# Kernel optimization log

Hardware: AMD Instinct MI355X
Metric: run time of the kernel (lower is better)

## Reference

```python
import jax, jax.numpy as jnp
import numpy as np

N = 50000       # nodes
E = 500000      # directed edges
Q_EDGES = 100000
F_IN = 128
HID = 64
K = 2           # Chebyshev order -> K+1 weight slices
LABEL = 2
Q_PHASE = 0.25
TWO_PI = 2.0 * np.pi


def setup_inputs() -> dict:
    key = jax.random.key(0)
    ks = jax.random.split(key, 9)
    real = jax.random.normal(ks[0], (N, F_IN), jnp.float32)
    imag = jax.random.normal(ks[1], (N, F_IN), jnp.float32)
    src = jax.random.randint(ks[2], (E,), 0, N)
    off = jax.random.randint(ks[3], (E,), 1, N)
    dst = (src + off) % N  # no self loops (torch code removes them)
    edge_index = jnp.stack([src, dst]).astype(jnp.int64)
    query_edges = jax.random.randint(ks[4], (Q_EDGES, 2), 0, N).astype(jnp.int64)
    edge_weight = jax.random.uniform(ks[5], (E,), jnp.float32, 0.5, 1.5)
    W1 = jax.random.normal(ks[6], (K + 1, F_IN, HID), jnp.float32) / np.sqrt(F_IN)
    b1 = jnp.zeros((HID,), jnp.float32)
    W2 = jax.random.normal(ks[7], (K + 1, HID, HID), jnp.float32) / np.sqrt(HID)
    b2 = jnp.zeros((HID,), jnp.float32)
    Wlin = jax.random.normal(ks[8], (LABEL, 4 * HID), jnp.float32) / np.sqrt(4 * HID)
    blin = jnp.zeros((LABEL,), jnp.float32)
    return dict(real=real, imag=imag, edge_index=edge_index, query_edges=query_edges,
                edge_weight=edge_weight, W1=W1, b1=b1, W2=W2, b2=b2, Wlin=Wlin, blin=blin)


def magnetic_norm(edge_index, edge_weight, num_nodes, q):
    """Edge weights of scaled magnetic Laplacian L_hat = L - I (sym norm, lambda_max=2).

    Returns symmetrized edge list (2E edges) with real/imag coefficients
    -D^{-1/2} A_s D^{-1/2} * exp(i * theta), theta = 2*pi*q*(A - A^T).
    """
    u, v = edge_index[0], edge_index[1]
    s = jnp.concatenate([u, v])                  # source (j)
    d = jnp.concatenate([v, u])                  # target (i)
    w_sym = jnp.concatenate([edge_weight, edge_weight]) * 0.5  # A_s = (A + A^T)/2
    theta = TWO_PI * q * jnp.concatenate([edge_weight, -edge_weight])
    deg = jax.ops.segment_sum(w_sym, s, num_segments=num_nodes)
    dinv = jnp.where(deg > 0, jax.lax.rsqrt(jnp.where(deg > 0, deg, 1.0)), 0.0)
    norm = dinv[s] * w_sym * dinv[d]
    return s, d, -norm * jnp.cos(theta), -norm * jnp.sin(theta)


def magnet_conv(xr, xi, s, d, nr, ni, W, b, num_nodes):
    def prop(x, c):  # out[i] = sum_{e: d_e = i} c_e * x[s_e]
        return jax.ops.segment_sum(c[:, None] * x[s], d, num_segments=num_nodes)

    xs = (xr, xi, xr, xi)            # streams: real_real, imag_imag, imag_real, real_imag
    cs = (nr, ni, ni, nr)            # norm used by each stream
    T0 = xs
    out = [x @ W[0] for x in T0]
    T1 = tuple(prop(x, c) for x, c in zip(xs, cs))
    out = [o + t @ W[1] for o, t in zip(out, T1)]
    for k in range(2, W.shape[0]):
        T2 = tuple(2.0 * prop(t1, c) - t0 for t0, t1, c in zip(T0, T1, cs))
        out = [o + t @ W[k] for o, t in zip(out, T2)]
        T0, T1 = T1, T2
    out_r = out[0] - out[1] + b
    out_i = out[2] + out[3] + b
    return out_r, out_i


def complex_relu(xr, xi):
    mask = (xr >= 0).astype(xr.dtype)
    return xr * mask, xi * mask


def reference(real, imag, edge_index, query_edges, edge_weight, W1, b1, W2, b2, Wlin, blin):
    num_nodes = real.shape[0]
    s, d, nr, ni = magnetic_norm(edge_index, edge_weight, num_nodes, Q_PHASE)
    xr, xi = magnet_conv(real, imag, s, d, nr, ni, W1, b1, num_nodes)
    xr, xi = complex_relu(xr, xi)
    xr, xi = magnet_conv(xr, xi, s, d, nr, ni, W2, b2, num_nodes)
    xr, xi = complex_relu(xr, xi)
    q0, q1 = query_edges[:, 0], query_edges[:, 1]
    x = jnp.concatenate([xr[q0], xr[q1], xi[q0], xi[q1]], axis=-1)  # [Q, 4*hidden]
    # dropout is identity in eval mode
    logits = x @ Wlin.T + blin
    return jax.nn.log_softmax(logits, axis=1)
```

## Files before the change

### kernel.cpp

```cpp
#include <hip/hip_runtime.h>


__device__ __forceinline__ float4 ld4(const float* __restrict__ p) {
  return *reinterpret_cast<const float4*>(p);
}
__device__ __forceinline__ float2 ld2(const float* __restrict__ p) {
  return *reinterpret_cast<const float2*>(p);
}

__global__ void k_deg_count(const int* __restrict__ u, const int* __restrict__ v,
                            const float* __restrict__ w,
                            unsigned long long* __restrict__ dc, int E) {
  int e = blockIdx.x * 256 + threadIdx.x;
  if (e >= E) return;
  float hw = 0.5f * w[e];
  unsigned fx = __float2uint_rn(hw * 16777216.f);
  unsigned long long pk = (1ULL << 32) | (unsigned long long)fx;
  atomicAdd(&dc[u[e]], pk);
  atomicAdd(&dc[v[e]], pk);
}

__global__ __launch_bounds__(256) void k_scan1(
    const unsigned long long* __restrict__ dc, int* __restrict__ rp,
    int* __restrict__ bsum, int N) {
  __shared__ int sh[256];
  int t = threadIdx.x;
  int base = blockIdx.x * 1024 + t * 4;
  int c0 = (base + 0 < N) ? (int)(dc[base + 0] >> 32) : 0;
  int c1 = (base + 1 < N) ? (int)(dc[base + 1] >> 32) : 0;
  int c2 = (base + 2 < N) ? (int)(dc[base + 2] >> 32) : 0;
  int c3 = (base + 3 < N) ? (int)(dc[base + 3] >> 32) : 0;
  int s = c0 + c1 + c2 + c3;
  sh[t] = s;
  __syncthreads();
  for (int o = 1; o < 256; o <<= 1) {
    int y = (t >= o) ? sh[t - o] : 0;
    __syncthreads();
    if (t >= o) sh[t] += y;
    __syncthreads();
  }
  int excl = sh[t] - s;
  if (base + 0 < N) rp[base + 0] = excl;
  if (base + 1 < N) rp[base + 1] = excl + c0;
  if (base + 2 < N) rp[base + 2] = excl + c0 + c1;
  if (base + 3 < N) rp[base + 3] = excl + c0 + c1 + c2;
  if (t == 255) bsum[blockIdx.x] = sh[255];
}

__global__ void k_scan2(int* __restrict__ bsum, int NB) {
  if (threadIdx.x == 0 && blockIdx.x == 0) {
    int run = 0;
    for (int i = 0; i < NB; ++i) { int x = bsum[i]; bsum[i] = run; run += x; }
  }
}

__global__ void k_scan3(int* __restrict__ rp, int* __restrict__ nxt,
                        const int* __restrict__ bsum, int N, int twoE) {
  int i = blockIdx.x * 256 + threadIdx.x;
  if (i < N) {
    int val = rp[i] + bsum[i >> 10];
    rp[i] = val;
    nxt[i] = val;
  } else if (i == N) {
    rp[N] = twoE;
  }
}

__global__ void k_scatter(const int* __restrict__ u, const int* __restrict__ v,
                          const float* __restrict__ w,
                          const unsigned long long* __restrict__ dc,
                          int* __restrict__ nxt, int* __restrict__ src,
                          float2* __restrict__ cf, int E) {
  int e = blockIdx.x * 256 + threadIdx.x;
  if (e >= E) return;
  int a = u[e], b = v[e];
  float we = w[e];
  float da = (float)(unsigned)dc[a] * (1.f / 16777216.f);
  float db = (float)(unsigned)dc[b] * (1.f / 16777216.f);
  float ia = da > 0.f ? rsqrtf(da) : 0.f;
  float ib = db > 0.f ? rsqrtf(db) : 0.f;
  float norm = ia * (0.5f * we) * ib;
  float th = 1.57079632679489662f * we;
  float sn, cs;
  sincosf(th, &sn, &cs);
  float cr = -norm * cs, ci = -norm * sn;
  int p1 = atomicAdd(&nxt[b], 1);
  src[p1] = a;
  cf[p1] = make_float2(cr, ci);
  int p2 = atomicAdd(&nxt[a], 1);
  src[p2] = b;
  cf[p2] = make_float2(cr, -ci);
}

template <int K>
__global__ __launch_bounds__(256) void k_gemmF(
    const float* __restrict__ Ar, const float* __restrict__ Ai,
    const float* __restrict__ W,
    const float* __restrict__ bias,
    float* __restrict__ P1, float* __restrict__ P2,
    float* __restrict__ Hr, float* __restrict__ Hi, int M) {
  __shared__ float Asr[32][36];
  __shared__ float Asi[32][36];
  __shared__ float Ws1[32][64];
  __shared__ float Ws2[32][64];
  __shared__ float Wsm[32][64];
  const int t = threadIdx.x;
  const int r0 = blockIdx.x * 32;
  const int tc = t & 15, tr = t >> 4;
  const float* W0 = W;
  const float* W1 = W + (size_t)K * 64;
  const float* W2 = W + (size_t)2 * K * 64;
  float a1r[2][4] = {}, a1i[2][4] = {}, a2r[2][4] = {}, a2i[2][4] = {};
  float amr[2][4] = {}, ami[2][4] = {};
  for (int k0 = 0; k0 < K; k0 += 32) {
    {
      int row = t >> 3, c4 = t & 7;
      int gr = r0 + row;
      float4 fr = make_float4(0.f, 0.f, 0.f, 0.f), fi = fr;
      if (gr < M) {
        fr = ld4(&Ar[(size_t)gr * K + k0 + c4 * 4]);
        fi = ld4(&Ai[(size_t)gr * K + k0 + c4 * 4]);
      }
      *reinterpret_cast<float4*>(&Asr[row][c4 * 4]) = fr;
      *reinterpret_cast<float4*>(&Asi[row][c4 * 4]) = fi;
    }
    for (int li = t; li < 512; li += 256) {
      int row = li >> 4, c4 = li & 15;
      size_t woff = (size_t)(k0 + row) * 64 + c4 * 4;
      float4 w1 = ld4(&W1[woff]);
      float4 w2 = ld4(&W2[woff]);
      float4 w0 = ld4(&W0[woff]);
      *reinterpret_cast<float4*>(&Ws1[row][c4 * 4]) = w1;
      *reinterpret_cast<float4*>(&Ws2[row][c4 * 4]) = w2;
      *reinterpret_cast<float4*>(&Wsm[row][c4 * 4]) =
          make_float4(w0.x - w2.x, w0.y - w2.y, w0.z - w2.z, w0.w - w2.w);
    }
    __syncthreads();
#pragma unroll 4
    for (int k = 0; k < 32; ++k) {
      float4 b1 = *reinterpret_cast<const float4*>(&Ws1[k][tc * 4]);
      float4 b2 = *reinterpret_cast<const float4*>(&Ws2[k][tc * 4]);
      float4 bm = *reinterpret_cast<const float4*>(&Wsm[k][tc * 4]);
#pragma unroll
      for (int i = 0; i < 2; ++i) {
        float ar = Asr[tr * 2 + i][k], ai = Asi[tr * 2 + i][k];
        a1r[i][0] += ar * b1.x; a1r[i][1] += ar * b1.y; a1r[i][2] += ar * b1.z; a1r[i][3] += ar * b1.w;
        a1i[i][0] += ai * b1.x; a1i[i][1] += ai * b1.y; a1i[i][2] += ai * b1.z; a1i[i][3] += ai * b1.w;
        a2r[i][0] += ar * b2.x; a2r[i][1] += ar * b2.y; a2r[i][2] += ar * b2.z; a2r[i][3] += ar * b2.w;
        a2i[i][0] += ai * b2.x; a2i[i][1] += ai * b2.y; a2i[i][2] += ai * b2.z; a2i[i][3] += ai * b2.w;
        amr[i][0] += ar * bm.x; amr[i][1] += ar * bm.y; amr[i][2] += ar * bm.z; amr[i][3] += ar * bm.w;
        ami[i][0] += ai * bm.x; ami[i][1] += ai * bm.y; ami[i][2] += ai * bm.z; ami[i][3] += ai * bm.w;
      }
    }
    __syncthreads();
  }
  float b0 = bias[tc * 4 + 0], bb1 = bias[tc * 4 + 1];
  float b2v = bias[tc * 4 + 2], b3 = bias[tc * 4 + 3];
#pragma unroll
  for (int i = 0; i < 2; ++i) {
    int gr = r0 + tr * 2 + i;
    if (gr >= M) continue;
    size_t pb = (size_t)gr * 128 + tc * 8;
    *reinterpret_cast<float4*>(&P1[pb]) =
        make_float4(a1r[i][0], a1i[i][0], a1r[i][1], a1i[i][1]);
    *reinterpret_cast<float4*>(&P1[pb + 4]) =
        make_float4(a1r[i][2], a1i[i][2], a1r[i][3], a1i[i][3]);
    *reinterpret_cast<float4*>(&P2[pb]) =
        make_float4(a2r[i][0], a2i[i][0], a2r[i][1], a2i[i][1]);
    *reinterpret_cast<float4*>(&P2[pb + 4]) =
        make_float4(a2r[i][2], a2i[i][2], a2r[i][3], a2i[i][3]);
    size_t hb = (size_t)gr * 64 + tc * 4;
    *reinterpret_cast<float4*>(&Hr[hb]) =
        make_float4(amr[i][0] - ami[i][0] + b0, amr[i][1] - ami[i][1] + bb1,
                    amr[i][2] - ami[i][2] + b2v, amr[i][3] - ami[i][3] + b3);
    *reinterpret_cast<float4*>(&Hi[hb]) =
        make_float4(amr[i][0] + ami[i][0] + b0, amr[i][1] + ami[i][1] + bb1,
                    amr[i][2] + ami[i][2] + b2v, amr[i][3] + ami[i][3] + b3);
  }
}

__global__ __launch_bounds__(256) void k_gU(
    const int* __restrict__ src, const float2* __restrict__ cf,
    const int* __restrict__ rp, const float* __restrict__ P2,
    const float* __restrict__ P1, float* __restrict__ Z, int N) {
  int d = blockIdx.x * 4 + (threadIdx.x >> 6);
  if (d >= N) return;
  int lane = threadIdx.x & 63;
  int g = lane >> 5, lg = lane & 31;
  float4 a01 = {0, 0, 0, 0};
  float4 a23 = {0, 0, 0, 0};
  int k1 = rp[d + 1];
#pragma unroll 2
  for (int k = rp[d] + g; k < k1; k += 2) {
    int s = src[k];
    float2 c = cf[k];
    float4 v = ld4(P2 + (size_t)s * 128 + lg * 4);
    a01.x += c.x * v.x; a01.y += c.y * v.y;
    a01.z += c.x * v.z; a01.w += c.y * v.w;
    a23.x += c.y * v.x; a23.y += c.x * v.y;
    a23.z += c.y * v.z; a23.w += c.x * v.w;
  }
  a01.x += __shfl_xor(a01.x, 32); a01.y += __shfl_xor(a01.y, 32);
  a01.z += __shfl_xor(a01.z, 32); a01.w += __shfl_xor(a01.w, 32);
  a23.x += __shfl_xor(a23.x, 32); a23.y += __shfl_xor(a23.y, 32);
  a23.z += __shfl_xor(a23.z, 32); a23.w += __shfl_xor(a23.w, 32);
  float4 p = ld4(P1 + (size_t)d * 128 + lg * 4);
  size_t zb = (size_t)d * 256 + lg * 4;
  if (g == 0)
    *reinterpret_cast<float4*>(&Z[zb]) =
        make_float4(p.x + 2.f * a01.x, p.y + 2.f * a01.y,
                    p.z + 2.f * a01.z, p.w + 2.f * a01.w);
  else
    *reinterpret_cast<float4*>(&Z[zb + 128]) =
        make_float4(p.x + 2.f * a23.x, p.y + 2.f * a23.y,
                    p.z + 2.f * a23.z, p.w + 2.f * a23.w);
}

__global__ __launch_bounds__(256) void k_gC(
    const int* __restrict__ src, const float2* __restrict__ cf,
    const int* __restrict__ rp, const float* __restrict__ Z,
    float* __restrict__ Hr, float* __restrict__ Hi, int N) {
  int d = blockIdx.x * 4 + (threadIdx.x >> 6);
  if (d >= N) return;
  int lane = threadIdx.x & 63;
  int g = lane >> 5, lg = lane & 31;
  float2 ahr = {0, 0}, ahi = {0, 0};
  int k1 = rp[d + 1];
#pragma unroll 2
  for (int k = rp[d] + g; k < k1; k += 2) {
    int s = src[k];
    float2 c = cf[k];
    const float* row = Z + (size_t)s * 256 + lg * 4;
    float4 z1 = ld4(row);
    float4 z2 = ld4(row + 128);
    ahr.x += c.x * z1.x - c.y * z1.y;
    ahr.y += c.x * z1.z - c.y * z1.w;
    ahi.x += c.y * z2.x + c.x * z2.y;
    ahi.y += c.y * z2.z + c.x * z2.w;
  }
  ahr.x += __shfl_xor(ahr.x, 32);
  ahr.y += __shfl_xor(ahr.y, 32);
  ahi.x += __shfl_xor(ahi.x, 32);
  ahi.y += __shfl_xor(ahi.y, 32);
  if (g == 0) {
    size_t hb = (size_t)d * 64 + lg * 2;
    float2 hr = ld2(&Hr[hb]);
    float2 hi = ld2(&Hi[hb]);
    hr.x += ahr.x; hr.y += ahr.y;
    hi.x += ahi.x; hi.y += ahi.y;
    if (hr.x < 0.f) { hr.x = 0.f; hi.x = 0.f; }
    if (hr.y < 0.f) { hr.y = 0.f; hi.y = 0.f; }
    *reinterpret_cast<float2*>(&Hr[hb]) = hr;
    *reinterpret_cast<float2*>(&Hi[hb]) = hi;
  }
}

__global__ __launch_bounds__(256) void k_query(
    const int* __restrict__ qe, const float* __restrict__ xr,
    const float* __restrict__ xi, const float* __restrict__ Wlin,
    const float* __restrict__ blin, float* __restrict__ out, int Q) {
  int q = blockIdx.x * 4 + (threadIdx.x >> 6);
  if (q >= Q) return;
  int lane = threadIdx.x & 63;
  int q0 = qe[2 * q], q1 = qe[2 * q + 1];
  float x0 = xr[(size_t)q0 * 64 + lane];
  float x1 = xr[(size_t)q1 * 64 + lane];
  float x2 = xi[(size_t)q0 * 64 + lane];
  float x3 = xi[(size_t)q1 * 64 + lane];
  float l0 = x0 * Wlin[lane] + x1 * Wlin[64 + lane] + x2 * Wlin[128 + lane] + x3 * Wlin[192 + lane];
  float l1 = x0 * Wlin[256 + lane] + x1 * Wlin[320 + lane] + x2 * Wlin[384 + lane] + x3 * Wlin[448 + lane];
#pragma unroll
  for (int o = 32; o > 0; o >>= 1) {
    l0 += __shfl_xor(l0, o);
    l1 += __shfl_xor(l1, o);
  }
  if (lane == 0) {
    l0 += blin[0];
    l1 += blin[1];
    float m = fmaxf(l0, l1);
    float lse = m + logf(expf(l0 - m) + expf(l1 - m));
    out[2 * q + 0] = l0 - lse;
    out[2 * q + 1] = l1 - lse;
  }
}

extern "C" void kernel_launch(void* const* d_in, const int* in_sizes, int n_in,
                              void* d_out, int out_size, void* d_ws, size_t ws_size,
                              hipStream_t stream) {
  const float* real = (const float*)d_in[0];
  const float* imag = (const float*)d_in[1];
  const int* ei     = (const int*)d_in[2];
  const int* qe     = (const int*)d_in[3];
  const float* ew   = (const float*)d_in[4];
  const float* W1   = (const float*)d_in[5];
  const float* b1   = (const float*)d_in[6];
  const float* W2   = (const float*)d_in[7];
  const float* b2   = (const float*)d_in[8];
  const float* Wlin = (const float*)d_in[9];
  const float* blin = (const float*)d_in[10];

  const int N = in_sizes[0] / 128;
  const int E = in_sizes[4];
  const int Q = in_sizes[3] / 2;
  const int* u = ei;
  const int* v = ei + E;

  float* ws = (float*)d_ws;
  size_t off = 0;
  auto alloc = [&](size_t n) { float* p = ws + off; off += n; return p; };
  const size_t N64 = (size_t)N * 64;
  const size_t N128 = (size_t)N * 128;
  const size_t N256 = (size_t)N * 256;

  float2* cf = (float2*)alloc((size_t)2 * E * 2);
  unsigned long long* dc = (unsigned long long*)alloc((size_t)2 * N);
  int* src  = (int*)alloc((size_t)2 * E);
  float* P1  = alloc(N128);
  float* P2  = alloc(N128);
  float* Z   = alloc(N256);
  float* HAr = alloc(N64);
  float* HAi = alloc(N64);
  float* HBr = alloc(N64);
  float* HBi = alloc(N64);
  int* rp   = (int*)alloc(N + 1);
  int* nxt  = (int*)alloc(N);
  int* bsum = (int*)alloc(64);
  (void)ws_size; (void)n_in; (void)out_size;

  const int eb = (E + 255) / 256;
  const int mb = (N + 31) / 32;
  const int NB = (N + 1023) / 1024;
  const int gb = (N + 3) / 4;

  hipMemsetAsync(dc, 0, (size_t)N * 8, stream);
  k_deg_count<<<eb, 256, 0, stream>>>(u, v, ew, dc, E);
  k_scan1<<<NB, 256, 0, stream>>>(dc, rp, bsum, N);
  k_scan2<<<1, 64, 0, stream>>>(bsum, NB);
  k_scan3<<<(N + 256) / 256, 256, 0, stream>>>(rp, nxt, bsum, N, 2 * E);
  k_scatter<<<eb, 256, 0, stream>>>(u, v, ew, dc, nxt, src, cf, E);

  k_gemmF<128><<<mb, 256, 0, stream>>>(real, imag, W1, b1, P1, P2, HAr, HAi, N);
  k_gU<<<gb, 256, 0, stream>>>(src, cf, rp, P2, P1, Z, N);
  k_gC<<<gb, 256, 0, stream>>>(src, cf, rp, Z, HAr, HAi, N);

  k_gemmF<64><<<mb, 256, 0, stream>>>(HAr, HAi, W2, b2, P1, P2, HBr, HBi, N);
  k_gU<<<gb, 256, 0, stream>>>(src, cf, rp, P2, P1, Z, N);
  k_gC<<<gb, 256, 0, stream>>>(src, cf, rp, Z, HBr, HBi, N);

  k_query<<<(Q + 3) / 4, 256, 0, stream>>>(qe, HBr, HBi, Wlin, blin, (float*)d_out, Q);
}
```

Before: 685.7 us.

## Fuse degree counting with first-layer GEMM and fold block-sum scan into scan3

Merges the edge degree-count atomics and the first-layer feature GEMM into one launch, with block ranges split between the two jobs, so the independent work overlaps on the device and one launch goes away. The separate single-thread block-sum scan kernel is also removed: each thread in scan3 now sums the preceding block totals itself. This cuts two kernel launches and serial gaps. The cost is redundant bsum reads per thread and a heavier shared-memory footprint on the degree-count blocks, which may reduce their occupancy.

Result: no change. 689.9 us (+0.6%).

```diff
diff --git a/kernel.cpp b/kernel.cpp
--- a/kernel.cpp
+++ b/kernel.cpp
@@ -8,95 +8,111 @@
   return *reinterpret_cast<const float2*>(p);
 }
 
-__global__ void k_deg_count(const int* __restrict__ u, const int* __restrict__ v,
-                            const float* __restrict__ w,
-                            unsigned long long* __restrict__ dc, int E) {
-  int e = blockIdx.x * 256 + threadIdx.x;
-  if (e >= E) return;
-  float hw = 0.5f * w[e];
-  unsigned fx = __float2uint_rn(hw * 16777216.f);
-  unsigned long long pk = (1ULL << 32) | (unsigned long long)fx;
-  atomicAdd(&dc[u[e]], pk);
-  atomicAdd(&dc[v[e]], pk);
-}
-
-__global__ __launch_bounds__(256) void k_scan1(
-    const unsigned long long* __restrict__ dc, int* __restrict__ rp,
-    int* __restrict__ bsum, int N) {
-  __shared__ int sh[256];
-  int t = threadIdx.x;
-  int base = blockIdx.x * 1024 + t * 4;
-  int c0 = (base + 0 < N) ? (int)(dc[base + 0] >> 32) : 0;
-  int c1 = (base + 1 < N) ? (int)(dc[base + 1] >> 32) : 0;
-  int c2 = (base + 2 < N) ? (int)(dc[base + 2] >> 32) : 0;
-  int c3 = (base + 3 < N) ? (int)(dc[base + 3] >> 32) : 0;
-  int s = c0 + c1 + c2 + c3;
-  sh[t] = s;
-  __syncthreads();
-  for (int o = 1; o < 256; o <<= 1) {
-    int y = (t >= o) ? sh[t - o] : 0;
-    __syncthreads();
-    if (t >= o) sh[t] += y;
-    __syncthreads();
-  }
-  int excl = sh[t] - s;
-  if (base + 0 < N) rp[base + 0] = excl;
-  if (base + 1 < N) rp[base + 1] = excl + c0;
-  if (base + 2 < N) rp[base + 2] = excl + c0 + c1;
-  if (base + 3 < N) rp[base + 3] = excl + c0 + c1 + c2;
-  if (t == 255) bsum[blockIdx.x] = sh[255];
-}
-
-__global__ void k_scan2(int* __restrict__ bsum, int NB) {
-  if (threadIdx.x == 0 && blockIdx.x == 0) {
-    int run = 0;
-    for (int i = 0; i < NB; ++i) { int x = bsum[i]; bsum[i] = run; run += x; }
-  }
-}
-
-__global__ void k_scan3(int* __restrict__ rp, int* __restrict__ nxt,
-                        const int* __restrict__ bsum, int N, int twoE) {
-  int i = blockIdx.x * 256 + threadIdx.x;
-  if (i < N) {
-    int val = rp[i] + bsum[i >> 10];
-    rp[i] = val;
-    nxt[i] = val;
-  } else if (i == N) {
-    rp[N] = twoE;
-  }
-}
-
-__global__ void k_scatter(const int* __restrict__ u, const int* __restrict__ v,
-                          const float* __restrict__ w,
-                          const unsigned long long* __restrict__ dc,
-                          int* __restrict__ nxt, int* __restrict__ src,
-                          float2* __restrict__ cf, int E) {
-  int e = blockIdx.x * 256 + threadIdx.x;
-  if (e >= E) return;
-  int a = u[e], b = v[e];
-  float we = w[e];
-  float da = (float)(unsigned)dc[a] * (1.f / 16777216.f);
-  float db = (float)(unsigned)dc[b] * (1.f / 16777216.f);
-  float ia = da > 0.f ? rsqrtf(da) : 0.f;
-  float ib = db > 0.f ? rsqrtf(db) : 0.f;
-  float norm = ia * (0.5f * we) * ib;
-  float th = 1.57079632679489662f * we;
-  float sn, cs;
-  sincosf(th, &sn, &cs);
-  float cr = -norm * cs, ci = -norm * sn;
-  int p1 = atomicAdd(&nxt[b], 1);
-  src[p1] = a;
-  cf[p1] = make_float2(cr, ci);
-  int p2 = atomicAdd(&nxt[a], 1);
-  src[p2] = b;
-  cf[p2] = make_float2(cr, -ci);
+template <int K>
+__global__ __launch_bounds__(256) void k_fuse_deg_gemm(
+    const int* __restrict__ u, const int* __restrict__ v,
+    const float* __restrict__ w, unsigned long long* __restrict__ dc, int E,
+    int ebN,
+    const float* __restrict__ Ar, const float* __restrict__ Ai,
+    const float* __restrict__ W,
+    const float* __restrict__ bias,
+    float* __restrict__ P1, float* __restrict__ P2,
+    float* __restrict__ Hr, float* __restrict__ Hi, int M) {
+  __shared__ float Asr[32][36];
+  __shared__ float Asi[32][36];
+  __shared__ float Ws1[32][64];
+  __shared__ float Ws2[32][64];
+  __shared__ float Wsm[32][64];
+  if (blockIdx.x < (unsigned)ebN) {
+    int e = blockIdx.x * 256 + threadIdx.x;
+    if (e >= E) return;
+    float hw = 0.5f * w[e];
+    unsigned fx = __float2uint_rn(hw * 16777216.f);
+    unsigned long long pk = (1ULL << 32) | (unsigned long long)fx;
+    atomicAdd(&dc[u[e]], pk);
+    atomicAdd(&dc[v[e]], pk);
+    return;
+  }
+  const int bx = blockIdx.x - ebN;
+  const int t = threadIdx.x;
+  const int r0 = bx * 32;
+  const int tc = t & 15, tr = t >> 4;
+  const float* W0 = W;
+  const float* W1 = W + (size_t)K * 64;
+  const float* W2 = W + (size_t)2 * K * 64;
+  float a1r[2][4] = {}, a1i[2][4] = {}, a2r[2][4] = {}, a2i[2][4] = {};
+  float amr[2][4] = {}, ami[2][4] = {};
+  for (int k0 = 0; k0 < K; k0 += 32) {
+    {
+      int row = t >> 3, c4 = t & 7;
+      int gr = r0 + row;
+      float4 fr = make_float4(0.f, 0.f, 0.f, 0.f), fi = fr;
+      if (gr < M) {
+        fr = ld4(&Ar[(size_t)gr * K + k0 + c4 * 4]);
+        fi = ld4(&Ai[(size_t)gr * K + k0 + c4 * 4]);
+      }
+      *reinterpret_cast<float4*>(&Asr[row][c4 * 4]) = fr;
+      *reinterpret_cast<float4*>(&Asi[row][c4 * 4]) = fi;
+    }
+    for (int li = t; li < 512; li += 256) {
+      int row = li >> 4, c4 = li & 15;
+      size_t woff = (size_t)(k0 + row) * 64 + c4 * 4;
+      float4 w1 = ld4(&W1[woff]);
+      float4 w2 = ld4(&W2[woff]);
+      float4 w0 = ld4(&W0[woff]);
+      *reinterpret_cast<float4*>(&Ws1[row][c4 * 4]) = w1;
+      *reinterpret_cast<float4*>(&Ws2[row][c4 * 4]) = w2;
+      *reinterpret_cast<float4*>(&Wsm[row][c4 * 4]) =
+          make_float4(w0.x - w2.x, w0.y - w2.y, w0.z - w2.z, w0.w - w2.w);
+    }
+    __syncthreads();
+#pragma unroll 4
+    for (int k = 0; k < 32; ++k) {
+      float4 b1 = *reinterpret_cast<const float4*>(&Ws1[k][tc * 4]);
+      float4 b2 = *reinterpret_cast<const float4*>(&Ws2[k][tc * 4]);
+      float4 bm = *reinterpret_cast<const float4*>(&Wsm[k][tc * 4]);
+#pragma unroll
+      for (int i = 0; i < 2; ++i) {
+        float ar = Asr[tr * 2 + i][k], ai = Asi[tr * 2 + i][k];
+        a1r[i][0] += ar * b1.x; a1r[i][1] += ar * b1.y; a1r[i][2] += ar * b1.z; a1r[i][3] += ar * b1.w;
+        a1i[i][0] += ai * b1.x; a1i[i][1] += ai * b1.y; a1i[i][2] += ai * b1.z; a1i[i][3] += ai * b1.w;
+        a2r[i][0] += ar * b2.x; a2r[i][1] += ar * b2.y; a2r[i][2] += ar * b2.z; a2r[i][3] += ar * b2.w;
+        a2i[i][0] += ai * b2.x; a2i[i][1] += ai * b2.y; a2i[i][2] += ai * b2.z; a2i[i][3] += ai * b2.w;
+        amr[i][0] += ar * bm.x; amr[i][1] += ar * bm.y; amr[i][2] += ar * bm.z; amr[i][3] += ar * bm.w;
+        ami[i][0] += ai * bm.x; ami[i][1] += ai * bm.y; ami[i][2] += ai * bm.z; ami[i][3] += ai * bm.w;
+      }
+    }
+    __syncthreads();
+  }
+  float b0 = bias[tc * 4 + 0], bb1 = bias[tc * 4 + 1];
+  float b2v = bias[tc * 4 + 2], b3 = bias[tc * 4 + 3];
+#pragma unroll
+  for (int i = 0; i < 2; ++i) {
+    int gr = r0 + tr * 2 + i;
+    if (gr >= M) continue;
+    size_t pb = (size_t)gr * 128 + tc * 8;
+    *reinterpret_cast<float4*>(&P1[pb]) =
+        make_float4(a1r[i][0], a1i[i][0], a1r[i][1], a1i[i][1]);
+    *reinterpret_cast<float4*>(&P1[pb + 4]) =
+        make_float4(a1r[i][2], a1i[i][2], a1r[i][3], a1i[i][3]);
+    *reinterpret_cast<float4*>(&P2[pb]) =
+        make_float4(a2r[i][0], a2i[i][0], a2r[i][1], a2i[i][1]);
+    *reinterpret_cast<float4*>(&P2[pb + 4]) =
+        make_float4(a2r[i][2], a2i[i][2], a2r[i][3], a2i[i][3]);
+    size_t hb = (size_t)gr * 64 + tc * 4;
+    *reinterpret_cast<float4*>(&Hr[hb]) =
+        make_float4(amr[i][0] - ami[i][0] + b0, amr[i][1] - ami[i][1] + bb1,
+                    amr[i][2] - ami[i][2] + b2v, amr[i][3] - ami[i][3] + b3);
+    *reinterpret_cast<float4*>(&Hi[hb]) =
+        make_float4(amr[i][0] + ami[i][0] + b0, amr[i][1] + ami[i][1] + bb1,
+                    amr[i][2] + ami[i][2] + b2v, amr[i][3] + ami[i][3] + b3);
+  }
 }
 
 template <int K>
 __global__ __launch_bounds__(256) void k_gemmF(
     const float* __restrict__ Ar, const float* __restrict__ Ai,
-    const float* __restrict__ W,
-    const float* __restrict__ bias,
+    const float* __restrict__ W, const float* __restrict__ bias,
     float* __restrict__ P1, float* __restrict__ P2,
     float* __restrict__ Hr, float* __restrict__ Hi, int M) {
   __shared__ float Asr[32][36];
@@ -179,6 +195,72 @@
   }
 }
 
+__global__ __launch_bounds__(256) void k_scan1(
+    const unsigned long long* __restrict__ dc, int* __restrict__ rp,
+    int* __restrict__ bsum, int N) {
+  __shared__ int sh[256];
+  int t = threadIdx.x;
+  int base = blockIdx.x * 1024 + t * 4;
+  int c0 = (base + 0 < N) ? (int)(dc[base + 0] >> 32) : 0;
+  int c1 = (base + 1 < N) ? (int)(dc[base + 1] >> 32) : 0;
+  int c2 = (base + 2 < N) ? (int)(dc[base + 2] >> 32) : 0;
+  int c3 = (base + 3 < N) ? (int)(dc[base + 3] >> 32) : 0;
+  int s = c0 + c1 + c2 + c3;
+  sh[t] = s;
+  __syncthreads();
+  for (int o = 1; o < 256; o <<= 1) {
+    int y = (t >= o) ? sh[t - o] : 0;
+    __syncthreads();
+    if (t >= o) sh[t] += y;
+    __syncthreads();
+  }
+  int excl = sh[t] - s;
+  if (base + 0 < N) rp[base + 0] = excl;
+  if (base + 1 < N) rp[base + 1] = excl + c0;
+  if (base + 2 < N) rp[base + 2] = excl + c0 + c1;
+  if (base + 3 < N) rp[base + 3] = excl + c0 + c1 + c2;
+  if (t == 255) bsum[blockIdx.x] = sh[255];
+}
+
+__global__ void k_scan3(int* __restrict__ rp, int* __restrict__ nxt,
+                        const int* __restrict__ bsum, int N, int twoE) {
+  int i = blockIdx.x * 256 + threadIdx.x;
+  if (i > N) return;
+  if (i == N) { rp[N] = twoE; return; }
+  int b = i >> 10;
+  int pre = 0;
+  for (int j = 0; j < b; ++j) pre += bsum[j];
+  int val = rp[i] + pre;
+  rp[i] = val;
+  nxt[i] = val;
+}
+
+__global__ void k_scatter(const int* __restrict__ u, const int* __restrict__ v,
+                          const float* __restrict__ w,
+                          const unsigned long long* __restrict__ dc,
+                          int* __restrict__ nxt, int* __restrict__ src,
+                          float2* __restrict__ cf, int E) {
+  int e = blockIdx.x * 256 + threadIdx.x;
+  if (e >= E) return;
+  int a = u[e], b = v[e];
+  float we = w[e];
+  float da = (float)(unsigned)dc[a] * (1.f / 16777216.f);
+  float db = (float)(unsigned)dc[b] * (1.f / 16777216.f);
+  float ia = da > 0.f ? rsqrtf(da) : 0.f;
+  float ib = db > 0.f ? rsqrtf(db) : 0.f;
+  float norm = ia * (0.5f * we) * ib;
+  float th = 1.57079632679489662f * we;
+  float sn, cs;
+  sincosf(th, &sn, &cs);
+  float cr = -norm * cs, ci = -norm * sn;
+  int p1 = atomicAdd(&nxt[b], 1);
+  src[p1] = a;
+  cf[p1] = make_float2(cr, ci);
+  int p2 = atomicAdd(&nxt[a], 1);
+  src[p2] = b;
+  cf[p2] = make_float2(cr, -ci);
+}
+
 __global__ __launch_bounds__(256) void k_gU(
     const int* __restrict__ src, const float2* __restrict__ cf,
     const int* __restrict__ rp, const float* __restrict__ P2,
@@ -333,13 +415,12 @@
   const int gb = (N + 3) / 4;
 
   hipMemsetAsync(dc, 0, (size_t)N * 8, stream);
-  k_deg_count<<<eb, 256, 0, stream>>>(u, v, ew, dc, E);
+  k_fuse_deg_gemm<128><<<eb + mb, 256, 0, stream>>>(
+      u, v, ew, dc, E, eb, real, imag, W1, b1, P1, P2, HAr, HAi, N);
   k_scan1<<<NB, 256, 0, stream>>>(dc, rp, bsum, N);
-  k_scan2<<<1, 64, 0, stream>>>(bsum, NB);
   k_scan3<<<(N + 256) / 256, 256, 0, stream>>>(rp, nxt, bsum, N, 2 * E);
   k_scatter<<<eb, 256, 0, stream>>>(u, v, ew, dc, nxt, src, cf, E);
 
-  k_gemmF<128><<<mb, 256, 0, stream>>>(real, imag, W1, b1, P1, P2, HAr, HAi, N);
   k_gU<<<gb, 256, 0, stream>>>(src, cf, rp, P2, P1, Z, N);
   k_gC<<<gb, 256, 0, stream>>>(src, cf, rp, Z, HAr, HAi, N);
 
```
